# Kernel optimization log

Hardware: AMD Instinct MI355X
Metric: run time of the kernel (lower is better)

Reference implementation:

```python
import jax, jax.numpy as jnp
import numpy as np

B, OUT, IN = 4096, 1024, 1024
BN_EPS = 1e-5


def setup_inputs() -> dict:
    key = jax.random.key(0)
    kx, k1, k2, k3 = jax.random.split(key, 4)
    # kaiming_uniform_ with a=sqrt(5): bound = sqrt(6 / ((1+a^2) * fan_in)) = 1/sqrt(fan_in)
    bound = 1.0 / np.sqrt(IN)
    x = jax.random.normal(kx, (B, IN), dtype=jnp.float32)
    c1 = jax.random.uniform(k1, (OUT, IN), jnp.float32, -bound, bound)
    c2 = jax.random.uniform(k2, (OUT, IN), jnp.float32, -bound, bound)
    c3 = jax.random.uniform(k3, (OUT, IN), jnp.float32, -bound, bound)
    bias = jnp.zeros((OUT, IN), jnp.float32)
    gamma = jnp.ones((OUT,), jnp.float32)   # BatchNorm1d weight
    beta = jnp.zeros((OUT,), jnp.float32)   # BatchNorm1d bias
    return {"x": x, "c1": c1, "c2": c2, "c3": c3, "bias": bias,
            "gamma": gamma, "beta": beta}


def reference(x, c1, c2, c3, bias, gamma, beta):
    # Fused polynomial 'matmul': out[b,o] = sum_i x*c1 + x^2*c2 + x^3*c3 + bias
    x2 = x * x
    x3 = x2 * x
    y = (jnp.einsum('bi,oi->bo', x, c1)
         + jnp.einsum('bi,oi->bo', x2, c2)
         + jnp.einsum('bi,oi->bo', x3, c3)
         + jnp.sum(bias, axis=1))  # bias reduced over in_features
    # BatchNorm1d (training mode: batch statistics, biased variance)
    mean = jnp.mean(y, axis=0)
    var = jnp.var(y, axis=0)
    return (y - mean) * jax.lax.rsqrt(var + BN_EPS) * gamma + beta
```

## Files before the change

### kernel.cpp

```cpp
#include <hip/hip_runtime.h>
#include <stdint.h>

#define B_ROWS 4096
#define OUTF   1024
#define INF    1024
#define KTOT   3072
#define BN_EPS 1e-5f
#define BM 128
#define BN 64
#define BK 32

typedef short  short8  __attribute__((ext_vector_type(8)));
typedef float  floatx4 __attribute__((ext_vector_type(4)));

struct alignas(8) s4 { short x, y, z, w; };

__device__ __forceinline__ short f2bf(float f) {
  union { float f; uint32_t u; } cv; cv.f = f;
  uint32_t u = cv.u;
  uint32_t r = (u + 0x7fffu + ((u >> 16) & 1u)) >> 16;
  return (short)r;
}

__device__ __forceinline__ void load_lds16(const void* g, void* l) {
  __builtin_amdgcn_global_load_lds(
      (const __attribute__((address_space(1))) uint32_t*)(uintptr_t)g,
      (__attribute__((address_space(3))) uint32_t*)(uint32_t)(uintptr_t)l,
      16, 0, 0);
}

__global__ void prep_all(const float4* __restrict__ x4,
                         const float4* __restrict__ c1, const float4* __restrict__ c2,
                         const float4* __restrict__ c3, const float* __restrict__ bias,
                         short* __restrict__ Xb, short* __restrict__ Wb,
                         float* __restrict__ biassum) {
  int b = blockIdx.x;
  if (b < 4096) {
    int idx = b * 256 + threadIdx.x;
    float4 v = x4[idx];
    int row = idx >> 8;
    int c   = (idx & 255) << 2;
    size_t base = (size_t)row * KTOT + c;
    s4 p1 = { f2bf(v.x), f2bf(v.y), f2bf(v.z), f2bf(v.w) };
    float ax = v.x * v.x, ay = v.y * v.y, az = v.z * v.z, aw = v.w * v.w;
    s4 p2 = { f2bf(ax), f2bf(ay), f2bf(az), f2bf(aw) };
    s4 p3 = { f2bf(ax * v.x), f2bf(ay * v.y), f2bf(az * v.z), f2bf(aw * v.w) };
    *(s4*)&Xb[base]        = p1;
    *(s4*)&Xb[base + 1024] = p2;
    *(s4*)&Xb[base + 2048] = p3;
  } else if (b < 5120) {
    int idx = (b - 4096) * 256 + threadIdx.x;
    int row = idx >> 8;
    int c   = (idx & 255) << 2;
    size_t base = (size_t)row * KTOT + c;
    float4 a = c1[idx], bb = c2[idx], d = c3[idx];
    s4 p1 = { f2bf(a.x),  f2bf(a.y),  f2bf(a.z),  f2bf(a.w)  };
    s4 p2 = { f2bf(bb.x), f2bf(bb.y), f2bf(bb.z), f2bf(bb.w) };
    s4 p3 = { f2bf(d.x),  f2bf(d.y),  f2bf(d.z),  f2bf(d.w)  };
    *(s4*)&Wb[base]        = p1;
    *(s4*)&Wb[base + 1024] = p2;
    *(s4*)&Wb[base + 2048] = p3;
  } else {
    int o = (b - 5120) * 4 + (threadIdx.x >> 6);
    int l = threadIdx.x & 63;
    const float4* bp = (const float4*)(bias + (size_t)o * INF);
    float s = 0.f;
    for (int i = l; i < 256; i += 64) { float4 v = bp[i]; s += v.x + v.y + v.z + v.w; }
    #pragma unroll
    for (int off = 32; off; off >>= 1) s += __shfl_down(s, off, 64);
    if (l == 0) biassum[o] = s;
  }
}

__global__ __launch_bounds__(256, 2) void gemm_poly(
    const short* __restrict__ Xb, const short* __restrict__ Wb,
    const float* __restrict__ biassum, float* __restrict__ Y,
    float* __restrict__ psum, float* __restrict__ psq) {
  __shared__ __align__(16) short As[BM * BK];
  __shared__ __align__(16) short Bs[BN * BK];
  __shared__ float colred[2][2][BN];
  const int tid  = threadIdx.x;
  const int lane = tid & 63;
  const int wave = tid >> 6;
  const int wr = wave >> 1;
  const int wc = wave & 1;
  const int row0 = blockIdx.y * BM;
  const int col0 = blockIdx.x * BN;
  const short* Ag = Xb + (size_t)row0 * KTOT;
  const short* Bg = Wb + (size_t)col0 * KTOT;
  const int frag_m = lane & 15;
  const int sel = lane >> 4;
  floatx4 acc[4][2] = {};

  const int ra0 = tid >> 2,        qa0 = tid & 3;
  const int ra1 = (256 + tid) >> 2, qa1 = tid & 3;
  const int coa0 = ((qa0 ^ ((ra0 >> 1) & 3)) << 3);
  const int coa1 = ((qa1 ^ ((ra1 >> 1) & 3)) << 3);
  const int rb = tid >> 2, qb = tid & 3;
  const int cob = ((qb ^ ((rb >> 1) & 3)) << 3);

  for (int kt = 0; kt < KTOT; kt += BK) {
    load_lds16(Ag + (size_t)ra0 * KTOT + kt + coa0, &As[tid * 8]);
    load_lds16(Ag + (size_t)ra1 * KTOT + kt + coa1, &As[(256 + tid) * 8]);
    load_lds16(Bg + (size_t)rb  * KTOT + kt + cob,  &Bs[tid * 8]);
    __syncthreads();
    short8 af[4], bfr[2];
    #pragma unroll
    for (int i = 0; i < 4; ++i) {
      int r = wr * 64 + i * 16 + frag_m;
      int qp = sel ^ ((r >> 1) & 3);
      af[i] = *(const short8*)&As[r * BK + qp * 8];
    }
    #pragma unroll
    for (int j = 0; j < 2; ++j) {
      int r = wc * 32 + j * 16 + frag_m;
      int qp = sel ^ ((r >> 1) & 3);
      bfr[j] = *(const short8*)&Bs[r * BK + qp * 8];
    }
    #pragma unroll
    for (int i = 0; i < 4; ++i)
      #pragma unroll
      for (int j = 0; j < 2; ++j)
        acc[i][j] = __builtin_amdgcn_mfma_f32_16x16x32_bf16(af[i], bfr[j], acc[i][j], 0, 0, 0);
    __syncthreads();
  }

  const int drow = (lane >> 4) << 2;
  const int dcol = lane & 15;
  float s[2] = {0.f, 0.f}, sq[2] = {0.f, 0.f};
  #pragma unroll
  for (int j = 0; j < 2; ++j) {
    int gc = col0 + wc * 32 + j * 16 + dcol;
    float bsv = biassum[gc];
    #pragma unroll
    for (int i = 0; i < 4; ++i) {
      int gr = row0 + wr * 64 + i * 16 + drow;
      #pragma unroll
      for (int r = 0; r < 4; ++r) {
        float v = acc[i][j][r] + bsv;
        Y[(size_t)(gr + r) * OUTF + gc] = v;
        s[j] += v; sq[j] += v * v;
      }
    }
  }
  #pragma unroll
  for (int j = 0; j < 2; ++j) {
    s[j]  += __shfl_xor(s[j], 16, 64);  s[j]  += __shfl_xor(s[j], 32, 64);
    sq[j] += __shfl_xor(sq[j], 16, 64); sq[j] += __shfl_xor(sq[j], 32, 64);
  }
  if (sel == 0) {
    #pragma unroll
    for (int j = 0; j < 2; ++j) {
      int cc = wc * 32 + j * 16 + dcol;
      colred[wr][0][cc] = s[j];
      colred[wr][1][cc] = sq[j];
    }
  }
  __syncthreads();
  if (tid < BN) {
    float ssum = colred[0][0][tid] + colred[1][0][tid];
    float ssq  = colred[0][1][tid] + colred[1][1][tid];
    psum[(size_t)blockIdx.y * OUTF + col0 + tid] = ssum;
    psq [(size_t)blockIdx.y * OUTF + col0 + tid] = ssq;
  }
}

__global__ void finalize(const float* __restrict__ psum, const float* __restrict__ psq,
                         const float* __restrict__ gamma, const float* __restrict__ beta,
                         float* __restrict__ scale, float* __restrict__ shift) {
  int t = blockIdx.x * blockDim.x + threadIdx.x;
  float s = 0.f, s2 = 0.f;
  for (int p = 0; p < 32; ++p) { s += psum[p * OUTF + t]; s2 += psq[p * OUTF + t]; }
  float mean = s * (1.0f / B_ROWS);
  float var  = s2 * (1.0f / B_ROWS) - mean * mean;
  float sc = gamma[t] * rsqrtf(var + BN_EPS);
  scale[t] = sc;
  shift[t] = beta[t] - mean * sc;
}

__global__ void bn_apply(float* __restrict__ Y, const float* __restrict__ scale,
                         const float* __restrict__ shift) {
  int idx = blockIdx.x * blockDim.x + threadIdx.x;
  float4 v = ((float4*)Y)[idx];
  int c = (idx & 255) << 2;
  v.x = v.x * scale[c]     + shift[c];
  v.y = v.y * scale[c + 1] + shift[c + 1];
  v.z = v.z * scale[c + 2] + shift[c + 2];
  v.w = v.w * scale[c + 3] + shift[c + 3];
  ((float4*)Y)[idx] = v;
}

extern "C" void kernel_launch(void* const* d_in, const int* in_sizes, int n_in,
                              void* d_out, int out_size, void* d_ws, size_t ws_size,
                              hipStream_t stream) {
  const float* x     = (const float*)d_in[0];
  const float* c1    = (const float*)d_in[1];
  const float* c2    = (const float*)d_in[2];
  const float* c3    = (const float*)d_in[3];
  const float* bias  = (const float*)d_in[4];
  const float* gamma = (const float*)d_in[5];
  const float* beta  = (const float*)d_in[6];
  float* out = (float*)d_out;
  char* ws = (char*)d_ws;

  short* Xb      = (short*)(ws);
  short* Wb      = (short*)(ws + 25165824);
  float* biassum = (float*)(ws + 31457280);
  float* psum    = (float*)(ws + 31461376);
  float* psq     = (float*)(ws + 31592448);
  float* scale   = (float*)(ws + 31723520);
  float* shift   = (float*)(ws + 31727616);

  prep_all<<<5376, 256, 0, stream>>>((const float4*)x, (const float4*)c1,
                                     (const float4*)c2, (const float4*)c3,
                                     bias, Xb, Wb, biassum);

  dim3 ggrid(OUTF / BN, B_ROWS / BM);
  gemm_poly<<<ggrid, 256, 0, stream>>>(Xb, Wb, biassum, out, psum, psq);

  finalize<<<4, 256, 0, stream>>>(psum, psq, gamma, beta, scale, shift);
  bn_apply<<<4096, 256, 0, stream>>>(out, scale, shift);
}
```

Before: 150.4 us.

## Deepen GEMM K-tile to 128 with wider swizzle and fuse BN finalize into apply

The GEMM K-tile grows from 32 to 128, so each block stages 8 A and 4 B 16-byte chunks per thread and runs four MFMA sub-steps between barriers, with a 16-way XOR swizzle to avoid LDS bank conflicts. This cuts the number of barrier round trips per tile, at the cost of more LDS per block (48KB), which may limit occupancy. The separate finalize and bn_apply kernels are merged into one kernel that computes scale/shift for 32 columns into shared memory and then applies them to a 256-row slab, removing one launch and the scale/shift round trip through global memory.

```diff
diff --git a/kernel.cpp b/kernel.cpp
--- a/kernel.cpp
+++ b/kernel.cpp
@@ -8,7 +8,7 @@
 #define BN_EPS 1e-5f
 #define BM 128
 #define BN 64
-#define BK 32
+#define BK 128
 
 typedef short  short8  __attribute__((ext_vector_type(8)));
 typedef float  floatx4 __attribute__((ext_vector_type(4)));
@@ -92,36 +92,51 @@
   const int sel = lane >> 4;
   floatx4 acc[4][2] = {};
 
-  const int ra0 = tid >> 2,        qa0 = tid & 3;
-  const int ra1 = (256 + tid) >> 2, qa1 = tid & 3;
-  const int coa0 = ((qa0 ^ ((ra0 >> 1) & 3)) << 3);
-  const int coa1 = ((qa1 ^ ((ra1 >> 1) & 3)) << 3);
-  const int rb = tid >> 2, qb = tid & 3;
-  const int cob = ((qb ^ ((rb >> 1) & 3)) << 3);
+  int aoff[8], boff[4];
+  #pragma unroll
+  for (int i = 0; i < 8; ++i) {
+    int c = tid + i * 256;
+    int r = c >> 4, p = c & 15;
+    int l = p ^ (r & 15);
+    aoff[i] = r * KTOT + l * 8;
+  }
+  #pragma unroll
+  for (int i = 0; i < 4; ++i) {
+    int c = tid + i * 256;
+    int r = c >> 4, p = c & 15;
+    int l = p ^ (r & 15);
+    boff[i] = r * KTOT + l * 8;
+  }
 
   for (int kt = 0; kt < KTOT; kt += BK) {
-    load_lds16(Ag + (size_t)ra0 * KTOT + kt + coa0, &As[tid * 8]);
-    load_lds16(Ag + (size_t)ra1 * KTOT + kt + coa1, &As[(256 + tid) * 8]);
-    load_lds16(Bg + (size_t)rb  * KTOT + kt + cob,  &Bs[tid * 8]);
+    #pragma unroll
+    for (int i = 0; i < 8; ++i)
+      load_lds16(Ag + aoff[i] + kt, &As[(tid + i * 256) * 8]);
+    #pragma unroll
+    for (int i = 0; i < 4; ++i)
+      load_lds16(Bg + boff[i] + kt, &Bs[(tid + i * 256) * 8]);
     __syncthreads();
-    short8 af[4], bfr[2];
-    #pragma unroll
-    for (int i = 0; i < 4; ++i) {
-      int r = wr * 64 + i * 16 + frag_m;
-      int qp = sel ^ ((r >> 1) & 3);
-      af[i] = *(const short8*)&As[r * BK + qp * 8];
-    }
-    #pragma unroll
-    for (int j = 0; j < 2; ++j) {
-      int r = wc * 32 + j * 16 + frag_m;
-      int qp = sel ^ ((r >> 1) & 3);
-      bfr[j] = *(const short8*)&Bs[r * BK + qp * 8];
-    }
-    #pragma unroll
-    for (int i = 0; i < 4; ++i)
-      #pragma unroll
-      for (int j = 0; j < 2; ++j)
-        acc[i][j] = __builtin_amdgcn_mfma_f32_16x16x32_bf16(af[i], bfr[j], acc[i][j], 0, 0, 0);
+    #pragma unroll
+    for (int s = 0; s < 4; ++s) {
+      short8 af[4], bfr[2];
+      #pragma unroll
+      for (int i = 0; i < 4; ++i) {
+        int r = wr * 64 + i * 16 + frag_m;
+        int p = (s * 4 + sel) ^ (r & 15);
+        af[i] = *(const short8*)&As[r * BK + p * 8];
+      }
+      #pragma unroll
+      for (int j = 0; j < 2; ++j) {
+        int r = wc * 32 + j * 16 + frag_m;
+        int p = (s * 4 + sel) ^ (r & 15);
+        bfr[j] = *(const short8*)&Bs[r * BK + p * 8];
+      }
+      #pragma unroll
+      for (int i = 0; i < 4; ++i)
+        #pragma unroll
+        for (int j = 0; j < 2; ++j)
+          acc[i][j] = __builtin_amdgcn_mfma_f32_16x16x32_bf16(af[i], bfr[j], acc[i][j], 0, 0, 0);
+    }
     __syncthreads();
   }
 
@@ -158,36 +173,47 @@
   }
   __syncthreads();
   if (tid < BN) {
-    float ssum = colred[0][0][tid] + colred[1][0][tid];
-    float ssq  = colred[0][1][tid] + colred[1][1][tid];
-    psum[(size_t)blockIdx.y * OUTF + col0 + tid] = ssum;
-    psq [(size_t)blockIdx.y * OUTF + col0 + tid] = ssq;
-  }
-}
-
-__global__ void finalize(const float* __restrict__ psum, const float* __restrict__ psq,
+    psum[(size_t)blockIdx.y * OUTF + col0 + tid] = colred[0][0][tid] + colred[1][0][tid];
+    psq [(size_t)blockIdx.y * OUTF + col0 + tid] = colred[0][1][tid] + colred[1][1][tid];
+  }
+}
+
+__global__ void bn_fused(const float* __restrict__ psum, const float* __restrict__ psq,
                          const float* __restrict__ gamma, const float* __restrict__ beta,
-                         float* __restrict__ scale, float* __restrict__ shift) {
-  int t = blockIdx.x * blockDim.x + threadIdx.x;
-  float s = 0.f, s2 = 0.f;
-  for (int p = 0; p < 32; ++p) { s += psum[p * OUTF + t]; s2 += psq[p * OUTF + t]; }
-  float mean = s * (1.0f / B_ROWS);
-  float var  = s2 * (1.0f / B_ROWS) - mean * mean;
-  float sc = gamma[t] * rsqrtf(var + BN_EPS);
-  scale[t] = sc;
-  shift[t] = beta[t] - mean * sc;
-}
-
-__global__ void bn_apply(float* __restrict__ Y, const float* __restrict__ scale,
-                         const float* __restrict__ shift) {
-  int idx = blockIdx.x * blockDim.x + threadIdx.x;
-  float4 v = ((float4*)Y)[idx];
-  int c = (idx & 255) << 2;
-  v.x = v.x * scale[c]     + shift[c];
-  v.y = v.y * scale[c + 1] + shift[c + 1];
-  v.z = v.z * scale[c + 2] + shift[c + 2];
-  v.w = v.w * scale[c + 3] + shift[c + 3];
-  ((float4*)Y)[idx] = v;
+                         float* __restrict__ Y) {
+  __shared__ float sc[32], sh[32];
+  const int c0 = blockIdx.x * 32;
+  const int t = threadIdx.x;
+  if (t < 32) {
+    float s = 0.f, s2 = 0.f;
+    #pragma unroll 8
+    for (int p = 0; p < 32; ++p) {
+      s  += psum[p * OUTF + c0 + t];
+      s2 += psq [p * OUTF + c0 + t];
+    }
+    float mean = s * (1.0f / B_ROWS);
+    float var  = s2 * (1.0f / B_ROWS) - mean * mean;
+    float scale = gamma[c0 + t] * rsqrtf(var + BN_EPS);
+    sc[t] = scale;
+    sh[t] = beta[c0 + t] - mean * scale;
+  }
+  __syncthreads();
+  const int f4c = t & 7;
+  const int rr  = t >> 3;
+  const int row0 = blockIdx.y * 256;
+  float4* Y4 = (float4*)Y;
+  const int cb = f4c * 4;
+  float s0 = sc[cb], s1 = sc[cb+1], s2 = sc[cb+2], s3 = sc[cb+3];
+  float h0 = sh[cb], h1 = sh[cb+1], h2 = sh[cb+2], h3 = sh[cb+3];
+  #pragma unroll
+  for (int it = 0; it < 8; ++it) {
+    int row = row0 + it * 32 + rr;
+    size_t idx = (size_t)row * 256 + (c0 >> 2) + f4c;
+    float4 v = Y4[idx];
+    v.x = v.x * s0 + h0; v.y = v.y * s1 + h1;
+    v.z = v.z * s2 + h2; v.w = v.w * s3 + h3;
+    Y4[idx] = v;
+  }
 }
 
 extern "C" void kernel_launch(void* const* d_in, const int* in_sizes, int n_in,
@@ -208,8 +234,6 @@
   float* biassum = (float*)(ws + 31457280);
   float* psum    = (float*)(ws + 31461376);
   float* psq     = (float*)(ws + 31592448);
-  float* scale   = (float*)(ws + 31723520);
-  float* shift   = (float*)(ws + 31727616);
 
   prep_all<<<5376, 256, 0, stream>>>((const float4*)x, (const float4*)c1,
                                      (const float4*)c2, (const float4*)c3,
@@ -218,6 +242,6 @@
   dim3 ggrid(OUTF / BN, B_ROWS / BM);
   gemm_poly<<<ggrid, 256, 0, stream>>>(Xb, Wb, biassum, out, psum, psq);
 
-  finalize<<<4, 256, 0, stream>>>(psum, psq, gamma, beta, scale, shift);
-  bn_apply<<<4096, 256, 0, stream>>>(out, scale, shift);
-}
+  dim3 bgrid(OUTF / 32, B_ROWS / 256);
+  bn_fused<<<bgrid, 256, 0, stream>>>(psum, psq, gamma, beta, out);
+}
```

Result: faster. 136.0 us (-9.6%).
